# Optimization experiments

Hardware: AMD Instinct MI355X
Metric: run time of the kernel (lower is better)

## Reference

```python
import jax, jax.numpy as jnp
import numpy as np

D_HEAD = 64


def setup_inputs() -> dict:
    key = jax.random.key(0)
    ks = jax.random.split(key, 9)
    B, S, D, H, Dh = 2, 2048, 1024, 16, D_HEAD
    scale = 0.02
    return {
        "normalized_resid_pre": jax.random.normal(ks[0], (B, S, D), jnp.float32),
        "W_Q": jax.random.normal(ks[1], (H, D, Dh), jnp.float32) * scale,
        "W_K": jax.random.normal(ks[2], (H, D, Dh), jnp.float32) * scale,
        "W_V": jax.random.normal(ks[3], (H, D, Dh), jnp.float32) * scale,
        "W_O": jax.random.normal(ks[4], (H, Dh, D), jnp.float32) * scale,
        "b_Q": jax.random.normal(ks[5], (H, Dh), jnp.float32) * scale,
        "b_K": jax.random.normal(ks[6], (H, Dh), jnp.float32) * scale,
        "b_V": jax.random.normal(ks[7], (H, Dh), jnp.float32) * scale,
        "b_O": jax.random.normal(ks[8], (D,), jnp.float32) * scale,
    }


def reference(normalized_resid_pre, W_Q, W_K, W_V, W_O, b_Q, b_K, b_V, b_O):
    x = normalized_resid_pre  # [b, s, d]
    IGNORE = jnp.float32(-1e5)
    q = jnp.einsum('bsd,hde->bshe', x, W_Q) + b_Q  # [b, s, h, dh]
    k = jnp.einsum('bsd,hde->bshe', x, W_K) + b_K
    v = jnp.einsum('bsd,hde->bshe', x, W_V) + b_V
    scores = jnp.einsum('bqhe,bkhe->bhqk', q, k) / jnp.sqrt(jnp.float32(D_HEAD))
    S = scores.shape[-1]
    causal = jnp.tril(jnp.ones((S, S), dtype=bool))  # True where allowed
    scores = jnp.where(causal, scores, IGNORE)
    pattern = jax.nn.softmax(scores, axis=-1)
    z = jnp.einsum('bkhe,bhqk->bqhe', v, pattern)
    attn_out = jnp.einsum('bqhe,hed->bqd', z, W_O) + b_O
    return attn_out
```

## Files before the change

### kernel.cpp

```cpp
#include <hip/hip_runtime.h>

typedef float f32x4 __attribute__((ext_vector_type(4)));
typedef __bf16 bf16x8_t __attribute__((ext_vector_type(8)));
typedef __bf16 bf16x4_t __attribute__((ext_vector_type(4)));
typedef unsigned int u32x2 __attribute__((ext_vector_type(2)));

#define GLOAD16(gptr, lptr)                                                        \
  __builtin_amdgcn_global_load_lds((const __attribute__((address_space(1))) void*)(gptr), \
                                   (__attribute__((address_space(3))) void*)(lptr), 16, 0, 0)

__device__ inline float fexp2(float x) {
  float r;
  asm("v_exp_f32 %0, %1" : "=v"(r) : "v"(x));
  return r;
}

union VFu { bf16x8_t v8; u32x2 w[2]; };

#define TRR(d, B, OFF) \
  asm volatile("ds_read_b64_tr_b16 %0, %1 offset:" OFF : "=v"(d) : "v"(B))

__global__ __launch_bounds__(256) void k_prep(const float* __restrict__ x,
                                              const float* __restrict__ wq,
                                              const float* __restrict__ wk,
                                              const float* __restrict__ wv,
                                              const float* __restrict__ wo,
                                              const float* __restrict__ bq,
                                              const float* __restrict__ bk,
                                              const float* __restrict__ bv,
                                              __bf16* __restrict__ xb,
                                              __bf16* __restrict__ wb1,
                                              __bf16* __restrict__ wb2,
                                              float* __restrict__ b1) {
  __shared__ __bf16 tr[64][64];
  int bid = blockIdx.x, t = threadIdx.x;
  if (bid < 4096) {
    int i = bid * 256 + t;
    float4 a = reinterpret_cast<const float4*>(x)[i];
    bf16x4_t o;
    o[0] = (__bf16)a.x; o[1] = (__bf16)a.y; o[2] = (__bf16)a.z; o[3] = (__bf16)a.w;
    reinterpret_cast<bf16x4_t*>(xb)[i] = o;
  } else if (bid < 4864) {
    int k = bid - 4096;
    int dt = k & 15, h = (k >> 4) & 15, p = k >> 8;
    const float* W = (p == 0) ? wq : (p == 1) ? wk : wv;
#pragma unroll
    for (int i = 0; i < 4; ++i) {
      int fl = i * 1024 + t * 4;
      int dd = fl >> 6, e = fl & 63;
      float4 a = *reinterpret_cast<const float4*>(W + ((size_t)(h * 1024 + dt * 64 + dd) * 64 + e));
      tr[e + 0][dd] = (__bf16)a.x; tr[e + 1][dd] = (__bf16)a.y;
      tr[e + 2][dd] = (__bf16)a.z; tr[e + 3][dd] = (__bf16)a.w;
    }
    __syncthreads();
#pragma unroll
    for (int i = 0; i < 2; ++i) {
      int ch = i * 256 + t;
      int e = ch >> 3, c8 = ch & 7;
      *reinterpret_cast<bf16x8_t*>(wb1 + ((size_t)(p * 1024 + h * 64 + e) * 1024 + dt * 64 + c8 * 8)) =
          *reinterpret_cast<const bf16x8_t*>(&tr[e][c8 * 8]);
    }
  } else if (bid < 5120) {
    int k = bid - 4864;
    int nt = k & 15, h = k >> 4;
#pragma unroll
    for (int i = 0; i < 4; ++i) {
      int fl = i * 1024 + t * 4;
      int e = fl >> 6, nn = fl & 63;
      float4 a = *reinterpret_cast<const float4*>(wo + ((size_t)(h * 64 + e) * 1024 + nt * 64 + nn));
      tr[nn + 0][e] = (__bf16)a.x; tr[nn + 1][e] = (__bf16)a.y;
      tr[nn + 2][e] = (__bf16)a.z; tr[nn + 3][e] = (__bf16)a.w;
    }
    __syncthreads();
#pragma unroll
    for (int i = 0; i < 2; ++i) {
      int ch = i * 256 + t;
      int nn = ch >> 3, c8 = ch & 7;
      *reinterpret_cast<bf16x8_t*>(wb2 + ((size_t)(nt * 64 + nn) * 1024 + h * 64 + c8 * 8)) =
          *reinterpret_cast<const bf16x8_t*>(&tr[nn][c8 * 8]);
    }
  } else {
    int n = (bid - 5120) * 256 + t;
    if (n < 3072) {
      int p = n >> 10, he = n & 1023;
      const float* s = (p == 0) ? bq : (p == 1) ? bk : bv;
      b1[n] = s[he];
    }
  }
}

template <typename OutT, int MODE, int MT, int NT>
__global__ __launch_bounds__(256) void k_gemm(const __bf16* __restrict__ A,
                                              const __bf16* __restrict__ Bt,
                                              const float* __restrict__ bias,
                                              OutT* __restrict__ C, int N, int K) {
  __shared__ __bf16 As[MT * 64];
  __shared__ __bf16 Bs[NT * 64];
  constexpr int MI = MT / 32;
  constexpr int NR = NT / 32;
  constexpr int AI = MT / 32;
  constexpr int BI = NT / 32;
  int t = threadIdx.x, l = t & 63;
  int lo = l & 15, hi = l >> 4;
  int w = t >> 6;
  int bid = blockIdx.x;
  int xcd = bid & 7, loc = bid >> 3;
  int xc = N / NT;
  int rx = (int)gridDim.x / (8 * xc);
  int yy = loc / xc;
  int xx = loc - yy * xc;
  int m0 = (xcd * rx + yy) * MT, n0 = xx * NT;
  int wm = (w >> 1) * (MT / 2), wn = (w & 1) * (NT / 2);
  f32x4 acc[MI][NR] = {};
  for (int k0 = 0; k0 < K; k0 += 64) {
    __syncthreads();
#pragma unroll
    for (int it = 0; it < AI; ++it) {
      int idx = it * 256 + t;
      int row = idx >> 3, c = idx & 7;
      int cs = (c ^ (row & 7)) * 8;
      GLOAD16(A + (size_t)(m0 + row) * K + k0 + cs, (char*)As + (it * 256 + (t & ~63)) * 16);
    }
#pragma unroll
    for (int it = 0; it < BI; ++it) {
      int idx = it * 256 + t;
      int row = idx >> 3, c = idx & 7;
      int cs = (c ^ (row & 7)) * 8;
      GLOAD16(Bt + (size_t)(n0 + row) * K + k0 + cs, (char*)Bs + (it * 256 + (t & ~63)) * 16);
    }
    __syncthreads();
#pragma unroll
    for (int kc = 0; kc < 2; ++kc) {
      bf16x8_t af[MI], bfr[NR];
#pragma unroll
      for (int mi = 0; mi < MI; ++mi) {
        int row = wm + mi * 16 + lo;
        af[mi] = *reinterpret_cast<const bf16x8_t*>(
            (char*)As + row * 128 + (((kc * 4 + hi) ^ (row & 7)) << 4));
      }
#pragma unroll
      for (int ni = 0; ni < NR; ++ni) {
        int row = wn + ni * 16 + lo;
        bfr[ni] = *reinterpret_cast<const bf16x8_t*>(
            (char*)Bs + row * 128 + (((kc * 4 + hi) ^ (row & 7)) << 4));
      }
#pragma unroll
      for (int mi = 0; mi < MI; ++mi)
#pragma unroll
        for (int ni = 0; ni < NR; ++ni)
          acc[mi][ni] = __builtin_amdgcn_mfma_f32_16x16x32_bf16(af[mi], bfr[ni], acc[mi][ni], 0, 0, 0);
    }
  }
  float qs = (MODE == 1 && n0 < 1024) ? 0.18033688f : 1.0f;
#pragma unroll
  for (int ni = 0; ni < NR; ++ni) {
    int n = n0 + wn + ni * 16 + lo;
    float bv = bias[n];
    int p = n >> 10, hh = (n >> 6) & 15, e = n & 63;
#pragma unroll
    for (int mi = 0; mi < MI; ++mi) {
#pragma unroll
      for (int r = 0; r < 4; ++r) {
        int m = m0 + wm + mi * 16 + hi * 4 + r;
        if (MODE == 0) {
          C[(size_t)m * N + n] = (OutT)(acc[mi][ni][r] + bv);
        } else {
          int b = m >> 11, sr = m & 2047;
          C[(size_t)(p * 32 + b * 16 + hh) * 131072 + sr * 64 + e] =
              (OutT)((acc[mi][ni][r] + bv) * qs);
        }
      }
    }
  }
}

__global__ __launch_bounds__(256, 4) void k_attn(const __bf16* __restrict__ QKVh,
                                                 __bf16* __restrict__ Z) {
  __shared__ __bf16 Ks[2][64 * 64];
  __shared__ __bf16 Vs[2][64 * 64];
  __shared__ __bf16 Ps[64 * 64];
  int t = threadIdx.x, l = t & 63, w = t >> 6;
  int lo = l & 15, hi = l >> 4;
  int bid = blockIdx.x;
  int xcd = bid & 7, kk = bid >> 3;
  int pr = kk & 15, bhl = kk >> 4;
  int bh = xcd * 4 + bhl;
  int b = bh >> 4, h = bh & 15;

  const __bf16* Qbase = QKVh + (size_t)bh * 131072;
  const __bf16* Kbase = QKVh + (size_t)(32 + bh) * 131072;
  const __bf16* Vbase = QKVh + (size_t)(64 + bh) * 131072;

  int kSrc[2], vSrc[2];
#pragma unroll
  for (int it = 0; it < 2; ++it) {
    int idx = it * 256 + t;
    int row = idx >> 3, c = idx & 7;
    kSrc[it] = row * 64 + ((c ^ (row & 7)) * 8);
    int kv = ((idx >> 1) & 3) | (((idx >> 5) & 1) << 2) | (((idx >> 3) & 3) << 3) |
             (((idx >> 8) & 1) << 5);
    int e0s = ((idx & 1) << 3) | (((idx >> 6) & 3) << 4);
    vSrc[it] = kv * 64 + e0s;
  }

#define STAGE_KV(buf, tile)                                                             \
  {                                                                                     \
    GLOAD16(Kbase + (tile) * 4096 + kSrc[0], (char*)Ks[buf] + (t & ~63) * 16);          \
    GLOAD16(Kbase + (tile) * 4096 + kSrc[1], (char*)Ks[buf] + 4096 + (t & ~63) * 16);   \
    GLOAD16(Vbase + (tile) * 4096 + vSrc[0], (char*)Vs[buf] + (t & ~63) * 16);          \
    GLOAD16(Vbase + (tile) * 4096 + vSrc[1], (char*)Vs[buf] + 4096 + (t & ~63) * 16);   \
  }

#pragma unroll 1
  for (int half = 0; half < 2; ++half) {
    int g = half ? pr : (31 - pr);
    int qbase = g * 64 + w * 16;
    int ntH = g + 1;

    bf16x8_t qf[2];
    {
      const __bf16* qptr = Qbase + (qbase + lo) * 64;
      qf[0] = *reinterpret_cast<const bf16x8_t*>(qptr + hi * 8);
      qf[1] = *reinterpret_cast<const bf16x8_t*>(qptr + 32 + hi * 8);
    }

    f32x4 zacc[4] = {};
    float lsum = 0.f;
    float mrow = -1e30f;

    STAGE_KV(0, 0);
    __syncthreads();

    for (int tile = 0; tile < ntH; ++tile) {
      int cur = tile & 1, kv0 = tile * 64;
      bool havenext = (tile + 1 < ntH);
      if (havenext) {
        STAGE_KV(cur ^ 1, tile + 1);
        __builtin_amdgcn_sched_barrier(0);
      }
      f32x4 s[4] = {};
      __builtin_amdgcn_s_setprio(1);
#pragma unroll
      for (int cb = 0; cb < 4; ++cb) {
        int krow = cb * 16 + lo;
        const char* kp = (const char*)Ks[cur] + krow * 128;
        bf16x8_t kf0 = *reinterpret_cast<const bf16x8_t*>(kp + ((hi ^ (krow & 7)) << 4));
        bf16x8_t kf1 = *reinterpret_cast<const bf16x8_t*>(kp + (((4 + hi) ^ (krow & 7)) << 4));
        s[cb] = __builtin_amdgcn_mfma_f32_16x16x32_bf16(kf0, qf[0], s[cb], 0, 0, 0);
        s[cb] = __builtin_amdgcn_mfma_f32_16x16x32_bf16(kf1, qf[1], s[cb], 0, 0, 0);
      }
      __builtin_amdgcn_s_setprio(0);
      {
        int qabs = qbase + lo;
        if (tile == ntH - 1) {
#pragma unroll
          for (int cb = 0; cb < 4; ++cb)
#pragma unroll
            for (int r = 0; r < 4; ++r)
              if (kv0 + cb * 16 + hi * 4 + r > qabs) s[cb][r] = -1e30f;
        }
        float mt = -1e30f;
#pragma unroll
        for (int cb = 0; cb < 4; ++cb) {
          float m01 = fmaxf(s[cb][0], s[cb][1]);
          float m23 = fmaxf(s[cb][2], s[cb][3]);
          mt = fmaxf(mt, fmaxf(m01, m23));
        }
        mt = fmaxf(mt, __shfl_xor(mt, 16));
        mt = fmaxf(mt, __shfl_xor(mt, 32));
        if (!__all(mt - mrow <= 8.0f)) {
          float mnew = fmaxf(mrow, mt);
          float alpha = fexp2(mrow - mnew);
          mrow = mnew;
          lsum *= alpha;
#pragma unroll
          for (int r = 0; r < 4; ++r) {
            float at = __shfl(alpha, hi * 4 + r);
#pragma unroll
            for (int e0 = 0; e0 < 4; ++e0) zacc[e0][r] *= at;
          }
        }
        float psum = 0.f;
        int prow = w * 16 + lo;
        char* prp = (char*)Ps + prow * 128 + (hi & 1) * 8;
        int rsw = prow & 7;
#pragma unroll
        for (int cb = 0; cb < 4; ++cb) {
          bf16x4_t pp;
#pragma unroll
          for (int r = 0; r < 4; ++r) {
            float p = fexp2(s[cb][r] - mrow);
            psum += p;
            pp[r] = (__bf16)p;
          }
          *reinterpret_cast<bf16x4_t*>(prp + (((cb * 2 + (hi >> 1)) ^ rsw) << 4)) = pp;
        }
        lsum += psum;
      }
      __builtin_amdgcn_s_setprio(1);
      {
        const __attribute__((address_space(3))) char* vb =
            (const __attribute__((address_space(3))) char*)((char*)Vs[cur]) + l * 8;
        int arow = w * 16 + lo;
        char* psb = (char*)Ps + arow * 128;
        const __attribute__((address_space(3))) char* pp0 =
            (const __attribute__((address_space(3))) char*)(psb + ((hi ^ (arow & 7)) << 4));
        const __attribute__((address_space(3))) char* pp1 =
            (const __attribute__((address_space(3))) char*)(psb + (((4 + hi) ^ (arow & 7)) << 4));
        bf16x8_t pf0, pf1;
        asm volatile("ds_read_b128 %0, %1" : "=v"(pf0) : "v"(pp0) : "memory");
        asm volatile("ds_read_b128 %0, %1" : "=v"(pf1) : "v"(pp1) : "memory");
        VFu u[8];
        TRR(u[0].w[0], vb, "0");    TRR(u[0].w[1], vb, "512");
        TRR(u[1].w[0], vb, "1024"); TRR(u[1].w[1], vb, "1536");
        TRR(u[2].w[0], vb, "2048"); TRR(u[2].w[1], vb, "2560");
        TRR(u[3].w[0], vb, "3072"); TRR(u[3].w[1], vb, "3584");
        TRR(u[4].w[0], vb, "4096"); TRR(u[4].w[1], vb, "4608");
        TRR(u[5].w[0], vb, "5120"); TRR(u[5].w[1], vb, "5632");
        TRR(u[6].w[0], vb, "6144"); TRR(u[6].w[1], vb, "6656");
        TRR(u[7].w[0], vb, "7168"); TRR(u[7].w[1], vb, "7680");
        asm volatile("s_waitcnt lgkmcnt(8)" ::: "memory");
        __builtin_amdgcn_sched_barrier(0);
        zacc[0] = __builtin_amdgcn_mfma_f32_16x16x32_bf16(pf0, u[0].v8, zacc[0], 0, 0, 0);
        zacc[1] = __builtin_amdgcn_mfma_f32_16x16x32_bf16(pf0, u[1].v8, zacc[1], 0, 0, 0);
        zacc[2] = __builtin_amdgcn_mfma_f32_16x16x32_bf16(pf0, u[2].v8, zacc[2], 0, 0, 0);
        zacc[3] = __builtin_amdgcn_mfma_f32_16x16x32_bf16(pf0, u[3].v8, zacc[3], 0, 0, 0);
        asm volatile("s_waitcnt lgkmcnt(0)" ::: "memory");
        __builtin_amdgcn_sched_barrier(0);
        zacc[0] = __builtin_amdgcn_mfma_f32_16x16x32_bf16(pf1, u[4].v8, zacc[0], 0, 0, 0);
        zacc[1] = __builtin_amdgcn_mfma_f32_16x16x32_bf16(pf1, u[5].v8, zacc[1], 0, 0, 0);
        zacc[2] = __builtin_amdgcn_mfma_f32_16x16x32_bf16(pf1, u[6].v8, zacc[2], 0, 0, 0);
        zacc[3] = __builtin_amdgcn_mfma_f32_16x16x32_bf16(pf1, u[7].v8, zacc[3], 0, 0, 0);
      }
      __builtin_amdgcn_s_setprio(0);
      __syncthreads();
    }

    float lt = lsum;
    lt += __shfl_xor(lt, 16);
    lt += __shfl_xor(lt, 32);
    float inv = 1.0f / lt;
#pragma unroll
    for (int r = 0; r < 4; ++r) {
      float lv = __shfl(inv, hi * 4 + r);
      size_t row = (size_t)(b * 2048 + qbase + hi * 4 + r);
#pragma unroll
      for (int e0 = 0; e0 < 4; ++e0)
        Z[row * 1024 + h * 64 + e0 * 16 + lo] = (__bf16)(zacc[e0][r] * lv);
    }
    __syncthreads();
  }
#undef STAGE_KV
}


extern "C" void kernel_launch(void* const* d_in, const int* in_sizes, int n_in,
                              void* d_out, int out_size, void* d_ws, size_t ws_size,
                              hipStream_t stream) {
  const float* x  = (const float*)d_in[0];
  const float* wq = (const float*)d_in[1];
  const float* wk = (const float*)d_in[2];
  const float* wv = (const float*)d_in[3];
  const float* wo = (const float*)d_in[4];
  const float* bq = (const float*)d_in[5];
  const float* bk = (const float*)d_in[6];
  const float* bv = (const float*)d_in[7];
  const float* bo = (const float*)d_in[8];
  float* out = (float*)d_out;

  char* ws = (char*)d_ws;
  __bf16* Xb   = (__bf16*)(ws);
  __bf16* WB1  = (__bf16*)(ws + 8388608);
  float*  B1   = (float*)(ws + 14680064);
  __bf16* WB2  = (__bf16*)(ws + 14692352);
  __bf16* QKVh = (__bf16*)(ws + 16789504);
  __bf16* Zb   = Xb;

  k_prep<<<5132, 256, 0, stream>>>(x, wq, wk, wv, wo, bq, bk, bv, Xb, WB1, WB2, B1);
  k_gemm<__bf16, 1, 128, 64><<<1536, 256, 0, stream>>>(Xb, WB1, B1, QKVh, 3072, 1024);
  k_attn<<<512, 256, 0, stream>>>(QKVh, Zb);
  k_gemm<float, 0, 64, 64><<<1024, 256, 0, stream>>>(Zb, WB2, bo, out, 1024, 1024);
}
```

Before: 115.6 us.

## Double-buffer GEMM shared-memory tiles with a 32-wide K step and prefetch

The bf16 GEMM kernel now splits its shared-memory A/B tiles into two buffers, each 32 wide in K instead of 64. The next K-slice is issued with global_load_lds while MFMAs run on the current one, leaving one barrier per iteration instead of two. The XOR swizzle is narrowed to 4 chunks to match the 64-byte rows. In exchange the loop runs twice as many iterations and barriers, each with less MFMA work. Small tile sizes could break the new load-count formulas.

```diff
diff --git a/kernel.cpp b/kernel.cpp
--- a/kernel.cpp
+++ b/kernel.cpp
@@ -94,12 +94,12 @@
                                               const __bf16* __restrict__ Bt,
                                               const float* __restrict__ bias,
                                               OutT* __restrict__ C, int N, int K) {
-  __shared__ __bf16 As[MT * 64];
-  __shared__ __bf16 Bs[NT * 64];
+  __shared__ __bf16 As[2][MT * 32];
+  __shared__ __bf16 Bs[2][NT * 32];
   constexpr int MI = MT / 32;
   constexpr int NR = NT / 32;
-  constexpr int AI = MT / 32;
-  constexpr int BI = NT / 32;
+  constexpr int AI = MT / 64;
+  constexpr int BI = NT / 64 > 0 ? NT / 64 : 1;
   int t = threadIdx.x, l = t & 63;
   int lo = l & 15, hi = l >> 4;
   int w = t >> 6;
@@ -112,45 +112,51 @@
   int m0 = (xcd * rx + yy) * MT, n0 = xx * NT;
   int wm = (w >> 1) * (MT / 2), wn = (w & 1) * (NT / 2);
   f32x4 acc[MI][NR] = {};
-  for (int k0 = 0; k0 < K; k0 += 64) {
-    __syncthreads();
-#pragma unroll
-    for (int it = 0; it < AI; ++it) {
-      int idx = it * 256 + t;
-      int row = idx >> 3, c = idx & 7;
-      int cs = (c ^ (row & 7)) * 8;
-      GLOAD16(A + (size_t)(m0 + row) * K + k0 + cs, (char*)As + (it * 256 + (t & ~63)) * 16);
-    }
-#pragma unroll
-    for (int it = 0; it < BI; ++it) {
-      int idx = it * 256 + t;
-      int row = idx >> 3, c = idx & 7;
-      int cs = (c ^ (row & 7)) * 8;
-      GLOAD16(Bt + (size_t)(n0 + row) * K + k0 + cs, (char*)Bs + (it * 256 + (t & ~63)) * 16);
-    }
-    __syncthreads();
-#pragma unroll
-    for (int kc = 0; kc < 2; ++kc) {
-      bf16x8_t af[MI], bfr[NR];
-#pragma unroll
-      for (int mi = 0; mi < MI; ++mi) {
-        int row = wm + mi * 16 + lo;
-        af[mi] = *reinterpret_cast<const bf16x8_t*>(
-            (char*)As + row * 128 + (((kc * 4 + hi) ^ (row & 7)) << 4));
-      }
-#pragma unroll
-      for (int ni = 0; ni < NR; ++ni) {
-        int row = wn + ni * 16 + lo;
-        bfr[ni] = *reinterpret_cast<const bf16x8_t*>(
-            (char*)Bs + row * 128 + (((kc * 4 + hi) ^ (row & 7)) << 4));
-      }
-#pragma unroll
-      for (int mi = 0; mi < MI; ++mi)
-#pragma unroll
-        for (int ni = 0; ni < NR; ++ni)
-          acc[mi][ni] = __builtin_amdgcn_mfma_f32_16x16x32_bf16(af[mi], bfr[ni], acc[mi][ni], 0, 0, 0);
-    }
-  }
+
+#define STAGE_G(buf, k0v)                                                               \
+  {                                                                                     \
+    _Pragma("unroll") for (int it = 0; it < AI; ++it) {                                 \
+      int idx = it * 256 + t;                                                           \
+      int row = idx >> 2, c = idx & 3;                                                  \
+      int cs = (c ^ (row & 3)) * 8;                                                     \
+      GLOAD16(A + (size_t)(m0 + row) * K + (k0v) + cs,                                  \
+              (char*)As[buf] + (it * 256 + (t & ~63)) * 16);                            \
+    }                                                                                   \
+    _Pragma("unroll") for (int it = 0; it < BI; ++it) {                                 \
+      int idx = it * 256 + t;                                                           \
+      int row = idx >> 2, c = idx & 3;                                                  \
+      int cs = (c ^ (row & 3)) * 8;                                                     \
+      GLOAD16(Bt + (size_t)(n0 + row) * K + (k0v) + cs,                                 \
+              (char*)Bs[buf] + (it * 256 + (t & ~63)) * 16);                            \
+    }                                                                                   \
+  }
+
+  STAGE_G(0, 0);
+  __syncthreads();
+  for (int k0 = 0; k0 < K; k0 += 32) {
+    int cur = (k0 >> 5) & 1;
+    if (k0 + 32 < K) STAGE_G(cur ^ 1, k0 + 32);
+    bf16x8_t af[MI], bfr[NR];
+#pragma unroll
+    for (int mi = 0; mi < MI; ++mi) {
+      int row = wm + mi * 16 + lo;
+      af[mi] = *reinterpret_cast<const bf16x8_t*>(
+          (char*)As[cur] + row * 64 + ((hi ^ (row & 3)) << 4));
+    }
+#pragma unroll
+    for (int ni = 0; ni < NR; ++ni) {
+      int row = wn + ni * 16 + lo;
+      bfr[ni] = *reinterpret_cast<const bf16x8_t*>(
+          (char*)Bs[cur] + row * 64 + ((hi ^ (row & 3)) << 4));
+    }
+#pragma unroll
+    for (int mi = 0; mi < MI; ++mi)
+#pragma unroll
+      for (int ni = 0; ni < NR; ++ni)
+        acc[mi][ni] = __builtin_amdgcn_mfma_f32_16x16x32_bf16(af[mi], bfr[ni], acc[mi][ni], 0, 0, 0);
+    __syncthreads();
+  }
+#undef STAGE_G
   float qs = (MODE == 1 && n0 < 1024) ? 0.18033688f : 1.0f;
 #pragma unroll
   for (int ni = 0; ni < NR; ++ni) {
```

Result: slower. 126.1 us (+9.1%).
